# Optimization experiments

Hardware: AMD Instinct MI355X
Metric: run time of the kernel (lower is better)

The kernel has to match this reference:

```python
import jax, jax.numpy as jnp
import numpy as np

R = 16
N = 65536
F = 2
MIN_RES, MAX_RES = 16, 512
SCALER = 1.0
M = 2097152
RESOLUTIONS = np.round(np.logspace(np.log2(MIN_RES), np.log2(MAX_RES), R, base=2)).astype(np.int32)
A = int(np.array(2654435761, dtype=np.uint32).view(np.int32))  # wraparound int32 constant


def _hash2d(xi, yi):
    # torch: bitwise_xor(x, 2654435761*y) % N  (int64). With N a power of 2,
    # low bits of the int32 wraparound product are identical, and & (N-1) == % N.
    return jnp.bitwise_and(jnp.bitwise_xor(xi, jnp.int32(A) * yi), N - 1)


def _bilerp_hash(coords, hash_features):
    res = jnp.asarray(RESOLUTIONS, jnp.float32)              # [R]
    xs = coords[None, :, :] * res[:, None, None]             # [R,M,2]
    x0 = jnp.floor(xs).astype(jnp.int32)
    w = xs - x0                                              # [R,M,2]
    wx, wy = w[..., :1], w[..., 1:]
    xi, yi = x0[..., 0], x0[..., 1]                          # [R,M]
    lvl = jnp.arange(R)[:, None]

    def gather(dx, dy):
        return hash_features[lvl, _hash2d(xi + dx, yi + dy)]  # [R,M,F]

    f = (gather(0, 0) * (1 - wx) * (1 - wy)
         + gather(0, 1) * (1 - wx) * wy
         + gather(1, 0) * wx * (1 - wy)
         + gather(1, 1) * wx * wy)
    scale = (2.0 ** (jnp.arange(R, dtype=jnp.float32) * SCALER))[:, None, None]
    f = f * scale                                            # per-level 2**(rix*scaler)
    return jnp.transpose(f, (1, 0, 2)).reshape(coords.shape[0], R * F)  # level-major concat


def _mlp(feats, w1, w2, w3):
    # tcnn FullyFusedMLP: 2 hidden ReLU layers of 32, sigmoid output, no bias
    h = jax.nn.relu(feats @ w1.T)
    h = jax.nn.relu(h @ w2.T)
    return jax.nn.sigmoid(h @ w3.T)


def setup_inputs() -> dict:
    key = jax.random.key(0)
    k0, k1, k2, k3, k4 = jax.random.split(key, 5)
    x = jax.random.uniform(k0, (M, 2), dtype=jnp.float32)
    hash_features = (jax.random.uniform(k1, (R, N, F), dtype=jnp.float32) - 0.5) * 0.0002
    w1 = jax.random.normal(k2, (32, R * F), dtype=jnp.float32) * 0.1
    w2 = jax.random.normal(k3, (32, 32), dtype=jnp.float32) * 0.1
    w3 = jax.random.normal(k4, (3, 32), dtype=jnp.float32) * 0.1
    return {"x": x, "hash_features": hash_features, "w1": w1, "w2": w2, "w3": w3}


def reference(x, hash_features, w1, w2, w3):
    feats = _bilerp_hash(x, hash_features)
    return _mlp(feats, w1, w2, w3)
```

## Files before the change

### kernel.cpp

```cpp
#include <hip/hip_runtime.h>
#include <math.h>


typedef _Float16 f16x8 __attribute__((ext_vector_type(8)));
typedef float    f32x4 __attribute__((ext_vector_type(4)));

static constexpr int RESC[16] = {16,20,25,32,40,51,64,81,102,128,161,203,256,323,406,512};
static constexpr int QOFF[12] = {0,256,656,1281,2305,3905,6506,10602,17163,27567,43951,69872};
static constexpr int QTOT = 111081;
static constexpr size_t QBYTES = (size_t)QTOT * 16;
static constexpr size_t WS_NEED = QBYTES + 4u * 65536u * 4u;
static constexpr int STRB = 80;

__device__ __forceinline__ float sigmoidf_(float a) { return 1.f / (1.f + __expf(-a)); }

__global__ __launch_bounds__(256) void build_tabs(
    const float2* __restrict__ hf,
    uint4* __restrict__ quad,
    unsigned* __restrict__ h16)
{
    const int l = blockIdx.y;
    const int e = blockIdx.x * 256 + threadIdx.x;
    if (l < 12) {
        const int res = RESC[l];
        const int n = res * res;
        if (e >= n) return;
        const int y = e / res;
        const int x = e - y * res;
        const unsigned ay0 = 2654435761u * (unsigned)y;
        const unsigned ay1 = 2654435761u * (unsigned)(y + 1);
        const int h00 = (int)(((unsigned)x       ^ ay0) & 65535u);
        const int h10 = (int)(((unsigned)(x + 1) ^ ay0) & 65535u);
        const int h01 = (int)(((unsigned)x       ^ ay1) & 65535u);
        const int h11 = (int)(((unsigned)(x + 1) ^ ay1) & 65535u);
        const float2* t = hf + l * 65536;
        const float2 f00 = t[h00], f10 = t[h10], f01 = t[h01], f11 = t[h11];
        union { _Float16 h[8]; uint4 u; } pk;
        pk.h[0] = (_Float16)f00.x; pk.h[1] = (_Float16)f00.y;
        pk.h[2] = (_Float16)f10.x; pk.h[3] = (_Float16)f10.y;
        pk.h[4] = (_Float16)f01.x; pk.h[5] = (_Float16)f01.y;
        pk.h[6] = (_Float16)f11.x; pk.h[7] = (_Float16)f11.y;
        quad[QOFF[l] + e] = pk.u;
    } else {
        if (e >= 65536) return;
        const float2 v = hf[l * 65536 + e];
        union { _Float16 h[2]; unsigned u; } pk;
        pk.h[0] = (_Float16)v.x; pk.h[1] = (_Float16)v.y;
        h16[(l - 12) * 65536 + e] = pk.u;
    }
}

__device__ __forceinline__ f16x8 load_wfrag(const float* __restrict__ w, int row, int g, bool valid) {
    f16x8 a;
    if (valid) {
        const float4 lo = *reinterpret_cast<const float4*>(w + row * 32 + g * 8);
        const float4 hi = *reinterpret_cast<const float4*>(w + row * 32 + g * 8 + 4);
        a[0]=(_Float16)lo.x; a[1]=(_Float16)lo.y; a[2]=(_Float16)lo.z; a[3]=(_Float16)lo.w;
        a[4]=(_Float16)hi.x; a[5]=(_Float16)hi.y; a[6]=(_Float16)hi.z; a[7]=(_Float16)hi.w;
    } else {
#pragma unroll
        for (int j = 0; j < 8; ++j) a[j] = (_Float16)0.f;
    }
    return a;
}

__global__ __launch_bounds__(256) void ngp_mfma2(
    const float2* __restrict__ x,
    const uint4*  __restrict__ quad,
    const unsigned* __restrict__ h16,
    const float*  __restrict__ w1,
    const float*  __restrict__ w2,
    const float*  __restrict__ w3,
    float* __restrict__ out)
{
    __shared__ char smem[4][64 * STRB];
    const int tid  = threadIdx.x;
    const int wv   = tid >> 6;
    const int lane = tid & 63;
    const int r    = lane & 15;
    const int g    = lane >> 4;
    char* sb = smem[wv];

    const int i = blockIdx.x * 256 + tid;
    const float2 c = x[i];

    uint4 q[12];
    float wxa[16], wya[16];
#pragma unroll
    for (int l = 0; l < 12; ++l) {
        const float rf = (float)RESC[l];
        const float xs = c.x * rf, ys = c.y * rf;
        const float fx = floorf(xs), fy = floorf(ys);
        wxa[l] = xs - fx; wya[l] = ys - fy;
        const int x0 = (int)fx, y0 = (int)fy;
        q[l] = quad[QOFF[l] + y0 * RESC[l] + x0];
    }
    unsigned u00[4], u01[4], u10[4], u11[4];
#pragma unroll
    for (int t = 0; t < 4; ++t) {
        const int l = 12 + t;
        const float rf = (float)RESC[l];
        const float xs = c.x * rf, ys = c.y * rf;
        const float fx = floorf(xs), fy = floorf(ys);
        wxa[l] = xs - fx; wya[l] = ys - fy;
        const int xi = (int)fx, yi = (int)fy;
        const unsigned ay0 = 2654435761u * (unsigned)yi;
        const unsigned ay1 = 2654435761u * (unsigned)(yi + 1);
        const unsigned* tb = h16 + t * 65536;
        u00[t] = tb[((unsigned)xi       ^ ay0) & 65535u];
        u01[t] = tb[((unsigned)xi       ^ ay1) & 65535u];
        u10[t] = tb[((unsigned)(xi + 1) ^ ay0) & 65535u];
        u11[t] = tb[((unsigned)(xi + 1) ^ ay1) & 65535u];
    }

    unsigned* srow = reinterpret_cast<unsigned*>(sb + lane * STRB);
#pragma unroll
    for (int l = 0; l < 12; ++l) {
        union { uint4 u; _Float16 h[8]; } pk; pk.u = q[l];
        const float wx = wxa[l], wy = wya[l];
        const float e0 = fmaf(wx, (float)pk.h[2] - (float)pk.h[0], (float)pk.h[0]);
        const float e1 = fmaf(wx, (float)pk.h[3] - (float)pk.h[1], (float)pk.h[1]);
        const float o0 = fmaf(wx, (float)pk.h[6] - (float)pk.h[4], (float)pk.h[4]);
        const float o1 = fmaf(wx, (float)pk.h[7] - (float)pk.h[5], (float)pk.h[5]);
        const float sc = (float)(1u << l);
        union { _Float16 h[2]; unsigned u; } o;
        o.h[0] = (_Float16)(fmaf(wy, o0 - e0, e0) * sc);
        o.h[1] = (_Float16)(fmaf(wy, o1 - e1, e1) * sc);
        srow[l] = o.u;
    }
#pragma unroll
    for (int t = 0; t < 4; ++t) {
        const int l = 12 + t;
        union { unsigned u; _Float16 h[2]; } a, b, cc, d;
        a.u = u00[t]; b.u = u10[t]; cc.u = u01[t]; d.u = u11[t];
        const float wx = wxa[l], wy = wya[l];
        const float e0 = fmaf(wx, (float)b.h[0] - (float)a.h[0], (float)a.h[0]);
        const float e1 = fmaf(wx, (float)b.h[1] - (float)a.h[1], (float)a.h[1]);
        const float o0 = fmaf(wx, (float)d.h[0] - (float)cc.h[0], (float)cc.h[0]);
        const float o1 = fmaf(wx, (float)d.h[1] - (float)cc.h[1], (float)cc.h[1]);
        const float sc = (float)(1u << l);
        union { _Float16 h[2]; unsigned u; } o;
        o.h[0] = (_Float16)(fmaf(wy, o0 - e0, e0) * sc);
        o.h[1] = (_Float16)(fmaf(wy, o1 - e1, e1) * sc);
        srow[l] = o.u;
    }

    f16x8 a1[2], a2[2], a3;
    a1[0] = load_wfrag(w1, r,      g, true);
    a1[1] = load_wfrag(w1, 16 + r, g, true);
    a2[0] = load_wfrag(w2, r,      g, true);
    a2[1] = load_wfrag(w2, 16 + r, g, true);
    a3    = load_wfrag(w3, r,      g, r < 3);

    const f32x4 zero = {0.f, 0.f, 0.f, 0.f};
    f16x8 bfr[4];

#pragma unroll
    for (int pt = 0; pt < 4; ++pt)
        bfr[pt] = *reinterpret_cast<const f16x8*>(sb + (pt * 16 + r) * STRB + g * 16);
#pragma unroll
    for (int nt = 0; nt < 2; ++nt) {
#pragma unroll
        for (int pt = 0; pt < 4; ++pt) {
            f32x4 acc = __builtin_amdgcn_mfma_f32_16x16x32_f16(a1[nt], bfr[pt], zero, 0, 0, 0);
            union { _Float16 h[4]; uint2 u; } pk;
#pragma unroll
            for (int qq = 0; qq < 4; ++qq) pk.h[qq] = (_Float16)fmaxf(acc[qq], 0.f);
            *reinterpret_cast<uint2*>(sb + (pt * 16 + r) * STRB + nt * 32 + g * 8) = pk.u;
        }
    }
#pragma unroll
    for (int pt = 0; pt < 4; ++pt)
        bfr[pt] = *reinterpret_cast<const f16x8*>(sb + (pt * 16 + r) * STRB + g * 16);
#pragma unroll
    for (int nt = 0; nt < 2; ++nt) {
#pragma unroll
        for (int pt = 0; pt < 4; ++pt) {
            f32x4 acc = __builtin_amdgcn_mfma_f32_16x16x32_f16(a2[nt], bfr[pt], zero, 0, 0, 0);
            union { _Float16 h[4]; uint2 u; } pk;
#pragma unroll
            for (int qq = 0; qq < 4; ++qq) pk.h[qq] = (_Float16)fmaxf(acc[qq], 0.f);
            *reinterpret_cast<uint2*>(sb + (pt * 16 + r) * STRB + nt * 32 + g * 8) = pk.u;
        }
    }
#pragma unroll
    for (int pt = 0; pt < 4; ++pt)
        bfr[pt] = *reinterpret_cast<const f16x8*>(sb + (pt * 16 + r) * STRB + g * 16);
#pragma unroll
    for (int pt = 0; pt < 4; ++pt) {
        f32x4 acc = __builtin_amdgcn_mfma_f32_16x16x32_f16(a3, bfr[pt], zero, 0, 0, 0);
        if (g == 0) {
            const int p = blockIdx.x * 256 + wv * 64 + pt * 16 + r;
            out[p * 3 + 0] = sigmoidf_(acc[0]);
            out[p * 3 + 1] = sigmoidf_(acc[1]);
            out[p * 3 + 2] = sigmoidf_(acc[2]);
        }
    }
}

__global__ __launch_bounds__(256) void ngp_tail(
    const float2* __restrict__ x, const float2* __restrict__ hf,
    const float* __restrict__ w1, const float* __restrict__ w2,
    const float* __restrict__ w3, float* __restrict__ out, int base, int M)
{
    const int i = base + blockIdx.x * 256 + threadIdx.x;
    if (i >= M) return;
    const float2 c = x[i];
    float feats[32];
#pragma unroll
    for (int l = 0; l < 16; ++l) {
        const float rf = (float)RESC[l];
        const float xs = c.x * rf, ys = c.y * rf;
        const float fx = floorf(xs), fy = floorf(ys);
        const int xi = (int)fx, yi = (int)fy;
        const float wx = xs - fx, wy = ys - fy;
        const unsigned ay0 = 2654435761u * (unsigned)yi;
        const unsigned ay1 = 2654435761u * (unsigned)(yi + 1);
        const int h00 = (int)(((unsigned)xi     ^ ay0) & 65535u);
        const int h01 = (int)(((unsigned)xi     ^ ay1) & 65535u);
        const int h10 = (int)(((unsigned)(xi+1) ^ ay0) & 65535u);
        const int h11 = (int)(((unsigned)(xi+1) ^ ay1) & 65535u);
        const float2* t = hf + l * 65536;
        const float2 f00 = t[h00], f01 = t[h01], f10 = t[h10], f11 = t[h11];
        const float e0 = fmaf(wx, f10.x - f00.x, f00.x);
        const float e1 = fmaf(wx, f10.y - f00.y, f00.y);
        const float o0 = fmaf(wx, f11.x - f01.x, f01.x);
        const float o1 = fmaf(wx, f11.y - f01.y, f01.y);
        const float sc = (float)(1u << l);
        feats[2*l]   = fmaf(wy, o0 - e0, e0) * sc;
        feats[2*l+1] = fmaf(wy, o1 - e1, e1) * sc;
    }
    float h1[32];
#pragma unroll
    for (int j = 0; j < 32; ++j) {
        float acc = 0.f;
#pragma unroll
        for (int k = 0; k < 32; ++k) acc = fmaf(feats[k], w1[j*32+k], acc);
        h1[j] = fmaxf(acc, 0.f);
    }
    float h2[32];
#pragma unroll
    for (int j = 0; j < 32; ++j) {
        float acc = 0.f;
#pragma unroll
        for (int k = 0; k < 32; ++k) acc = fmaf(h1[k], w2[j*32+k], acc);
        h2[j] = fmaxf(acc, 0.f);
    }
#pragma unroll
    for (int o = 0; o < 3; ++o) {
        float acc = 0.f;
#pragma unroll
        for (int k = 0; k < 32; ++k) acc = fmaf(h2[k], w3[o*32+k], acc);
        out[3*i + o] = 1.f / (1.f + __expf(-acc));
    }
}

extern "C" void kernel_launch(void* const* d_in, const int* in_sizes, int n_in,
                              void* d_out, int out_size, void* d_ws, size_t ws_size,
                              hipStream_t stream) {
    const float2* x  = (const float2*)d_in[0];
    const float2* hf = (const float2*)d_in[1];
    const float*  w1 = (const float*)d_in[2];
    const float*  w2 = (const float*)d_in[3];
    const float*  w3 = (const float*)d_in[4];
    float* out = (float*)d_out;
    const int M = in_sizes[0] / 2;

    if (ws_size >= WS_NEED) {
        uint4*    quad = (uint4*)d_ws;
        unsigned* h16  = (unsigned*)((char*)d_ws + QBYTES);
        build_tabs<<<dim3(256, 16), 256, 0, stream>>>(hf, quad, h16);
        const int full = M / 256;
        if (full > 0)
            ngp_mfma2<<<full, 256, 0, stream>>>(x, quad, h16, w1, w2, w3, out);
        const int base = full * 256;
        if (M - base > 0)
            ngp_tail<<<((M - base) + 255) / 256, 256, 0, stream>>>(x, hf, w1, w2, w3, out, base, M);
    } else {
        ngp_tail<<<(M + 255) / 256, 256, 0, stream>>>(x, hf, w1, w2, w3, out, 0, M);
    }
}
```

Baseline: 248.2 us.

## Bin points spatially via counting sort before hash-grid MLP kernel

Adds a histogram, a scan and a scatter pass that counting-sort point indices into a 64x64 spatial grid, so each wavefront processes spatially nearby points. The goal is cache locality for the table gathers in the main kernel. The main kernel reads coordinates through the sorted index and writes outputs back to the original positions via the index kept in shared memory. This adds three extra kernels plus a memset, heavy atomics on the scatter, and scattered output writes.

Result: slower. 353.3 us (+42.3%).

```diff
diff --git a/kernel.cpp b/kernel.cpp
--- a/kernel.cpp
+++ b/kernel.cpp
@@ -9,22 +9,29 @@
 static constexpr int QOFF[12] = {0,256,656,1281,2305,3905,6506,10602,17163,27567,43951,69872};
 static constexpr int QTOT = 111081;
 static constexpr size_t QBYTES = (size_t)QTOT * 16;
-static constexpr size_t WS_NEED = QBYTES + 4u * 65536u * 4u;
+static constexpr size_t OFF_H16  = 1777408;
+static constexpr size_t OFF_HIST = OFF_H16 + 1048576;
+static constexpr size_t OFF_CUR  = OFF_HIST + 16384;
+static constexpr size_t OFF_SID  = OFF_CUR + 16384;
+static constexpr int NB = 4096;
 static constexpr int STRB = 80;
 
 __device__ __forceinline__ float sigmoidf_(float a) { return 1.f / (1.f + __expf(-a)); }
 
+__device__ __forceinline__ int bin_of(float2 c) {
+    int bx = (int)(c.x * 64.f); bx = bx > 63 ? 63 : bx;
+    int by = (int)(c.y * 64.f); by = by > 63 ? 63 : by;
+    return by * 64 + bx;
+}
+
 __global__ __launch_bounds__(256) void build_tabs(
-    const float2* __restrict__ hf,
-    uint4* __restrict__ quad,
-    unsigned* __restrict__ h16)
+    const float2* __restrict__ hf, uint4* __restrict__ quad, unsigned* __restrict__ h16)
 {
     const int l = blockIdx.y;
     const int e = blockIdx.x * 256 + threadIdx.x;
     if (l < 12) {
         const int res = RESC[l];
-        const int n = res * res;
-        if (e >= n) return;
+        if (e >= res * res) return;
         const int y = e / res;
         const int x = e - y * res;
         const unsigned ay0 = 2654435761u * (unsigned)y;
@@ -50,6 +57,52 @@
     }
 }
 
+__global__ __launch_bounds__(256) void hist_bins(
+    const float2* __restrict__ x, int* __restrict__ hist, int M)
+{
+    __shared__ int lh[NB];
+    for (int t = threadIdx.x; t < NB; t += 256) lh[t] = 0;
+    __syncthreads();
+    for (int i = blockIdx.x * 256 + threadIdx.x; i < M; i += gridDim.x * 256)
+        atomicAdd(&lh[bin_of(x[i])], 1);
+    __syncthreads();
+    for (int t = threadIdx.x; t < NB; t += 256) {
+        const int v = lh[t];
+        if (v) atomicAdd(&hist[t], v);
+    }
+}
+
+__global__ __launch_bounds__(1024) void scan_bins(
+    const int* __restrict__ hist, int* __restrict__ cursor)
+{
+    __shared__ int ls[1024];
+    const int t = threadIdx.x;
+    const int h0 = hist[4*t], h1 = hist[4*t+1], h2 = hist[4*t+2], h3 = hist[4*t+3];
+    const int s = h0 + h1 + h2 + h3;
+    ls[t] = s;
+    __syncthreads();
+    for (int off = 1; off < 1024; off <<= 1) {
+        const int v = (t >= off) ? ls[t - off] : 0;
+        __syncthreads();
+        ls[t] += v;
+        __syncthreads();
+    }
+    const int excl = ls[t] - s;
+    cursor[4*t]   = excl;
+    cursor[4*t+1] = excl + h0;
+    cursor[4*t+2] = excl + h0 + h1;
+    cursor[4*t+3] = excl + h0 + h1 + h2;
+}
+
+__global__ __launch_bounds__(256) void scatter_pts(
+    const float2* __restrict__ x, int* __restrict__ cursor, int* __restrict__ sid, int M)
+{
+    const int i = blockIdx.x * 256 + threadIdx.x;
+    if (i >= M) return;
+    const int pos = atomicAdd(&cursor[bin_of(x[i])], 1);
+    sid[pos] = i;
+}
+
 __device__ __forceinline__ f16x8 load_wfrag(const float* __restrict__ w, int row, int g, bool valid) {
     f16x8 a;
     if (valid) {
@@ -64,13 +117,13 @@
     return a;
 }
 
-__global__ __launch_bounds__(256) void ngp_mfma2(
+template<int SORTED>
+__global__ __launch_bounds__(256) void ngp_mfma3(
     const float2* __restrict__ x,
+    const int*    __restrict__ sid,
     const uint4*  __restrict__ quad,
     const unsigned* __restrict__ h16,
-    const float*  __restrict__ w1,
-    const float*  __restrict__ w2,
-    const float*  __restrict__ w3,
+    const float*  __restrict__ w1, const float* __restrict__ w2, const float* __restrict__ w3,
     float* __restrict__ out)
 {
     __shared__ char smem[4][64 * STRB];
@@ -81,8 +134,10 @@
     const int g    = lane >> 4;
     char* sb = smem[wv];
 
-    const int i = blockIdx.x * 256 + tid;
-    const float2 c = x[i];
+    const int slot = blockIdx.x * 256 + tid;
+    const int id = SORTED ? sid[slot] : slot;
+    const float2 c = x[id];
+    *reinterpret_cast<int*>(sb + lane * STRB + 64) = id;
 
     uint4 q[12];
     float wxa[16], wya[16];
@@ -92,8 +147,7 @@
         const float xs = c.x * rf, ys = c.y * rf;
         const float fx = floorf(xs), fy = floorf(ys);
         wxa[l] = xs - fx; wya[l] = ys - fy;
-        const int x0 = (int)fx, y0 = (int)fy;
-        q[l] = quad[QOFF[l] + y0 * RESC[l] + x0];
+        q[l] = quad[QOFF[l] + (int)fy * RESC[l] + (int)fx];
     }
     unsigned u00[4], u01[4], u10[4], u11[4];
 #pragma unroll
@@ -154,7 +208,6 @@
 
     const f32x4 zero = {0.f, 0.f, 0.f, 0.f};
     f16x8 bfr[4];
-
 #pragma unroll
     for (int pt = 0; pt < 4; ++pt)
         bfr[pt] = *reinterpret_cast<const f16x8*>(sb + (pt * 16 + r) * STRB + g * 16);
@@ -190,15 +243,15 @@
     for (int pt = 0; pt < 4; ++pt) {
         f32x4 acc = __builtin_amdgcn_mfma_f32_16x16x32_f16(a3, bfr[pt], zero, 0, 0, 0);
         if (g == 0) {
-            const int p = blockIdx.x * 256 + wv * 64 + pt * 16 + r;
-            out[p * 3 + 0] = sigmoidf_(acc[0]);
-            out[p * 3 + 1] = sigmoidf_(acc[1]);
-            out[p * 3 + 2] = sigmoidf_(acc[2]);
+            const int idp = *reinterpret_cast<const int*>(sb + (pt * 16 + r) * STRB + 64);
+            out[idp * 3 + 0] = sigmoidf_(acc[0]);
+            out[idp * 3 + 1] = sigmoidf_(acc[1]);
+            out[idp * 3 + 2] = sigmoidf_(acc[2]);
         }
     }
 }
 
-__global__ __launch_bounds__(256) void ngp_tail(
+__global__ __launch_bounds__(256) void ngp_scalar(
     const float2* __restrict__ x, const float2* __restrict__ hf,
     const float* __restrict__ w1, const float* __restrict__ w2,
     const float* __restrict__ w3, float* __restrict__ out, int base, int M)
@@ -266,17 +319,32 @@
     float* out = (float*)d_out;
     const int M = in_sizes[0] / 2;
 
-    if (ws_size >= WS_NEED) {
-        uint4*    quad = (uint4*)d_ws;
-        unsigned* h16  = (unsigned*)((char*)d_ws + QBYTES);
+    const size_t ws_sort = OFF_SID + (size_t)M * 4;
+    const size_t ws_tabs = OFF_HIST;
+
+    if (ws_size >= ws_tabs) {
+        uint4*    quad   = (uint4*)d_ws;
+        unsigned* h16    = (unsigned*)((char*)d_ws + OFF_H16);
         build_tabs<<<dim3(256, 16), 256, 0, stream>>>(hf, quad, h16);
+
         const int full = M / 256;
-        if (full > 0)
-            ngp_mfma2<<<full, 256, 0, stream>>>(x, quad, h16, w1, w2, w3, out);
         const int base = full * 256;
-        if (M - base > 0)
-            ngp_tail<<<((M - base) + 255) / 256, 256, 0, stream>>>(x, hf, w1, w2, w3, out, base, M);
+        if (ws_size >= ws_sort && base == M) {
+            int* hist   = (int*)((char*)d_ws + OFF_HIST);
+            int* cursor = (int*)((char*)d_ws + OFF_CUR);
+            int* sid    = (int*)((char*)d_ws + OFF_SID);
+            hipMemsetAsync(hist, 0, NB * sizeof(int), stream);
+            hist_bins<<<64, 256, 0, stream>>>(x, hist, M);
+            scan_bins<<<1, 1024, 0, stream>>>(hist, cursor);
+            scatter_pts<<<(M + 255) / 256, 256, 0, stream>>>(x, cursor, sid, M);
+            ngp_mfma3<1><<<full, 256, 0, stream>>>(x, sid, quad, h16, w1, w2, w3, out);
+        } else {
+            if (full > 0)
+                ngp_mfma3<0><<<full, 256, 0, stream>>>(x, nullptr, quad, h16, w1, w2, w3, out);
+            if (M - base > 0)
+                ngp_scalar<<<((M - base) + 255) / 256, 256, 0, stream>>>(x, hf, w1, w2, w3, out, base, M);
+        }
     } else {
-        ngp_tail<<<(M + 255) / 256, 256, 0, stream>>>(x, hf, w1, w2, w3, out, 0, M);
-    }
-}
+        ngp_scalar<<<(M + 255) / 256, 256, 0, stream>>>(x, hf, w1, w2, w3, out, 0, M);
+    }
+}
```
